# Performance work log

Hardware: AMD Instinct MI355X
Metric: run time of the kernel (lower is better)

The kernel has to match this reference:

```python
import jax, jax.numpy as jnp
import numpy as np

HIDDEN = 1024
HEADS = 16
HEAD_DIM = HIDDEN // HEADS


def setup_inputs() -> dict:
    key = jax.random.key(0)
    ks = jax.random.split(key, 9)
    s = 1.0 / np.sqrt(HIDDEN)
    x = jax.random.normal(ks[0], (2, 2048, HIDDEN), dtype=jnp.float32)
    Wq = jax.random.uniform(ks[1], (HIDDEN, HIDDEN), jnp.float32, -s, s)
    bq = jax.random.uniform(ks[2], (HIDDEN,), jnp.float32, -s, s)
    Wk = jax.random.uniform(ks[3], (HIDDEN, HIDDEN), jnp.float32, -s, s)
    bk = jax.random.uniform(ks[4], (HIDDEN,), jnp.float32, -s, s)
    Wv = jax.random.uniform(ks[5], (HIDDEN, HIDDEN), jnp.float32, -s, s)
    bv = jax.random.uniform(ks[6], (HIDDEN,), jnp.float32, -s, s)
    Wo = jax.random.uniform(ks[7], (HIDDEN, HIDDEN), jnp.float32, -s, s)
    bo = jax.random.uniform(ks[8], (HIDDEN,), jnp.float32, -s, s)
    return {"x": x, "Wq": Wq, "bq": bq, "Wk": Wk, "bk": bk,
            "Wv": Wv, "bv": bv, "Wo": Wo, "bo": bo}


def reference(x, Wq, bq, Wk, bk, Wv, bv, Wo, bo):
    bs, seq_len, _ = x.shape
    # projections; weights stored as (in, out) so y = x @ W + b
    def proj(W, b):
        y = x @ W + b  # [bs, seq, hidden]
        return y.reshape(bs, seq_len, HEADS, HEAD_DIM).transpose(0, 2, 1, 3)  # [bs, h, seq, hd]
    q = proj(Wq, bq)
    k = proj(Wk, bk)
    v = proj(Wv, bv)
    scale = 1.0 / jnp.sqrt(jnp.float32(HEAD_DIM))
    scores = jnp.einsum('bhqd,bhkd->bhqk', q, k) * scale  # [bs, h, seq, seq]
    attn = jax.nn.softmax(scores, axis=-1)
    ctx = jnp.einsum('bhqk,bhkd->bhqd', attn, v)
    ctx = ctx.transpose(0, 2, 1, 3).reshape(bs, seq_len, HIDDEN)
    return ctx @ Wo + bo
```

## Files before the change

### kernel.cpp

```cpp
#include <hip/hip_runtime.h>
#include <hip/hip_bf16.h>

#define HDN 1024
#define NH  16
#define DH  64
#define NB  2
#define SQL 2048
#define MT  (NB*SQL)

using bf16 = __hip_bfloat16;
typedef __attribute__((ext_vector_type(8))) short s16x8;
typedef __attribute__((ext_vector_type(4))) float f32x4;
typedef __attribute__((ext_vector_type(16))) float f32x16;
typedef unsigned int u32;

#define QSC 0.18033688011112042f

__device__ __forceinline__ void gload_lds16(const void* g, void* l) {
  __builtin_amdgcn_global_load_lds((const __attribute__((address_space(1))) void*)g,
                                   (__attribute__((address_space(3))) void*)l, 16, 0, 0);
}

__device__ __forceinline__ unsigned short bfb(float f) {
  union { __hip_bfloat16 h; unsigned short u; } c;
  c.h = __float2bfloat16(f);
  return c.u;
}

__device__ __forceinline__ u32 cvtpk(float lo, float hi) {
  u32 r;
  asm("v_cvt_pk_bf16_f32 %0, %1, %2" : "=v"(r) : "v"(lo), "v"(hi));
  return r;
}

__device__ __forceinline__ void pl32swap(u32& a, u32& b) {
  asm("v_permlane32_swap_b32 %0, %1" : "+v"(a), "+v"(b));
}

__global__ __launch_bounds__(256) void k_cvt_x(const float* __restrict__ x, bf16* __restrict__ xb) {
  int i = (blockIdx.x * 256 + threadIdx.x) * 8;
  float4 a = *(const float4*)(x + i);
  float4 b = *(const float4*)(x + i + 4);
  union { unsigned short u[8]; uint4 v; } o;
  o.u[0]=bfb(a.x); o.u[1]=bfb(a.y); o.u[2]=bfb(a.z); o.u[3]=bfb(a.w);
  o.u[4]=bfb(b.x); o.u[5]=bfb(b.y); o.u[6]=bfb(b.z); o.u[7]=bfb(b.w);
  *(uint4*)((unsigned short*)xb + i) = o.v;
}

__global__ __launch_bounds__(256) void k_trw(const float* __restrict__ Wq, const float* __restrict__ Wk,
                                             const float* __restrict__ Wv, const float* __restrict__ Wo,
                                             bf16* __restrict__ WqkvT, bf16* __restrict__ WoT) {
  __shared__ float tile[64][65];
  int z = blockIdx.z;
  const float* W = (z==0)?Wq:(z==1)?Wk:(z==2)?Wv:Wo;
  bf16* Wt = (z<3) ? (WqkvT + (size_t)z*HDN*HDN) : WoT;
  int r0 = blockIdx.y*64, c0 = blockIdx.x*64;
  int t = threadIdx.x, tr = t>>4, tc = (t&15)*4;
  #pragma unroll
  for (int p=0;p<4;p++){
    int r = p*16+tr;
    float4 v = *(const float4*)(W + (size_t)(r0+r)*HDN + c0 + tc);
    tile[r][tc]=v.x; tile[r][tc+1]=v.y; tile[r][tc+2]=v.z; tile[r][tc+3]=v.w;
  }
  __syncthreads();
  #pragma unroll
  for (int p=0;p<4;p++){
    int o = p*16+tr;
    union { unsigned short u[4]; ushort4 v; } pk;
    #pragma unroll
    for (int j=0;j<4;j++) pk.u[j] = bfb(tile[tc+j][o]);
    *(ushort4*)((unsigned short*)Wt + (size_t)(c0+o)*HDN + r0 + tc) = pk.v;
  }
}

template<int MODE>
__global__ __launch_bounds__(256,2) void k_gemm(
    const bf16* __restrict__ A, const bf16* __restrict__ B,
    const float* __restrict__ b0, const float* __restrict__ b1, const float* __restrict__ b2,
    bf16* __restrict__ oq, bf16* __restrict__ ok, bf16* __restrict__ ovt, float* __restrict__ oo) {
  constexpr int KD = 1024;
  __shared__ __align__(16) bf16 As[128*64];
  __shared__ __align__(16) bf16 Bs[128*64];
  int tid = threadIdx.x, lane = tid&63, wave = tid>>6;
  int g = lane>>4, lr = lane&15;
  int m0 = blockIdx.y*128, n0 = blockIdx.x*128;
  int wm = (wave>>1)*64, wn = (wave&1)*64;
  f32x4 acc[4][4] = {};
  for (int k0=0; k0<KD; k0+=64) {
    #pragma unroll
    for (int i=0;i<4;i++){
      int seg = wave*4+i;
      int flat = seg*64 + lane;
      int row = flat>>3, ch = flat&7;
      gload_lds16(A + (size_t)(m0+row)*KD + k0 + ch*8, (char*)As + seg*1024);
      gload_lds16(B + (size_t)(n0+row)*KD + k0 + ch*8, (char*)Bs + seg*1024);
    }
    __syncthreads();
    #pragma unroll
    for (int kk=0;kk<2;kk++){
      s16x8 af[4], bfg[4];
      #pragma unroll
      for (int mi=0;mi<4;mi++)
        af[mi] = *(const s16x8*)((const char*)As + (wm+mi*16+lr)*128 + kk*64 + g*16);
      #pragma unroll
      for (int ni=0;ni<4;ni++)
        bfg[ni] = *(const s16x8*)((const char*)Bs + (wn+ni*16+lr)*128 + kk*64 + g*16);
      #pragma unroll
      for (int mi=0;mi<4;mi++)
        #pragma unroll
        for (int ni=0;ni<4;ni++)
          acc[mi][ni] = __builtin_amdgcn_mfma_f32_16x16x32_bf16(af[mi], bfg[ni], acc[mi][ni], 0,0,0);
    }
    __syncthreads();
  }
  if (MODE == 0) {
    int proj = n0 >> 10;
    const float* bias = (proj==0)?b0:(proj==1)?b1:b2;
    bf16* oqk = (proj==0)?oq:ok;
    float qscale = (proj==0) ? QSC : 1.0f;
    #pragma unroll
    for (int ni=0;ni<4;ni++){
      int n = n0 + wn + ni*16 + lr;
      int wi = n & 1023;
      int h = wi>>6, d = wi&63;
      float bv = bias[wi];
      #pragma unroll
      for (int mi=0;mi<4;mi++){
        #pragma unroll
        for (int r=0;r<4;r++){
          int m = m0 + wm + mi*16 + g*4 + r;
          int b = m>>11, s = m&2047;
          float v = (acc[mi][ni][r] + bv) * qscale;
          if (proj<2) oqk[((size_t)((b*NH+h)*SQL + s))*DH + d] = __float2bfloat16(v);
          else        ovt[((size_t)((b*NH+h)*DH  + d))*SQL + s] = __float2bfloat16(v);
        }
      }
    }
  } else {
    #pragma unroll
    for (int ni=0;ni<4;ni++){
      int n = n0 + wn + ni*16 + lr;
      float bv = b0[n];
      #pragma unroll
      for (int mi=0;mi<4;mi++)
        #pragma unroll
        for (int r=0;r<4;r++){
          int m = m0 + wm + mi*16 + g*4 + r;
          oo[(size_t)m*HDN + n] = acc[mi][ni][r] + bv;
        }
    }
  }
}

__global__ __launch_bounds__(512,4) void k_attn(
    const bf16* __restrict__ Q, const bf16* __restrict__ K, const bf16* __restrict__ Vt,
    bf16* __restrict__ ctx) {
  __shared__ __align__(16) char sm[2][2][16384];
  int bh = blockIdx.x & 31, qt = blockIdx.x >> 5;
  int b = bh >> 4, h = bh & 15;
  int tid = threadIdx.x;
  int kc = tid >> 8, tl = tid & 255;
  int w4 = tl >> 6;
  int lane = tid & 63;
  int cl = lane & 31, hi = lane >> 5;
  const char* Kc = (const char*)(K  + (size_t)bh*SQL*DH);
  const char* Vc = (const char*)(Vt + (size_t)bh*DH*SQL);
  const bf16* Qb = Q + (size_t)bh*SQL*DH;

  int L0 = tl*16, L1 = 4096 + tl*16;
  int r0 = L0>>7, c0 = (L0&127) ^ ((r0&7)<<4);
  int r1 = L1>>7, c1 = (L1&127) ^ ((r1&7)<<4);
  size_t kOff0 = (size_t)r0*128  + c0, kOff1 = (size_t)r1*128  + c1;
  size_t vOff0 = (size_t)r0*4096 + c0, vOff1 = (size_t)r1*4096 + c1;

  int swz = (cl&7)<<4;
  int cswz0 = (0*32 + hi*16) ^ swz;
  int cswz1 = (1*32 + hi*16) ^ swz;
  int cswz2 = (2*32 + hi*16) ^ swz;
  int cswz3 = (3*32 + hi*16) ^ swz;
  int rbase0 = cl*128;
  int rbase1 = (32+cl)*128;

  int q0 = qt*128 + w4*32;
  s16x8 qf[4];
  #pragma unroll
  for (int ds=0; ds<4; ++ds)
    qf[ds] = *(const s16x8*)((const char*)Qb + (size_t)(q0+cl)*128 + ds*32 + hi*16);

  s16x8 onef;
  #pragma unroll
  for (int i=0;i<8;i++) onef[i] = (short)0x3F80;

  f32x16 ca0 = {}, ca1 = {}, lacc = {};

  auto STAGE = [&](int bb, int t){
    int k0 = kc*1024 + t*64;
    char* bK = &sm[kc][bb][0]; char* bV = bK + 8192;
    gload_lds16(Kc + (size_t)k0*128 + kOff0, bK + w4*1024);
    gload_lds16(Kc + (size_t)k0*128 + kOff1, bK + 4096 + w4*1024);
    gload_lds16(Vc + (size_t)k0*2   + vOff0, bV + w4*1024);
    gload_lds16(Vc + (size_t)k0*2   + vOff1, bV + 4096 + w4*1024);
  };

  STAGE(0, 0);
  __syncthreads();

  for (int t=0; t<16; ++t){
    int cur = t & 1;
    if (t < 15) STAGE(cur^1, t+1);
    const char* bK = &sm[kc][cur][0];
    const char* bV = bK + 8192;

    f32x16 s0 = {}, s1 = {};
    {
      s16x8 k00 = *(const s16x8*)(bK + rbase0 + cswz0);
      s16x8 k10 = *(const s16x8*)(bK + rbase1 + cswz0);
      s0 = __builtin_amdgcn_mfma_f32_32x32x16_bf16(k00, qf[0], s0, 0,0,0);
      s1 = __builtin_amdgcn_mfma_f32_32x32x16_bf16(k10, qf[0], s1, 0,0,0);
      s16x8 k01 = *(const s16x8*)(bK + rbase0 + cswz1);
      s16x8 k11 = *(const s16x8*)(bK + rbase1 + cswz1);
      s0 = __builtin_amdgcn_mfma_f32_32x32x16_bf16(k01, qf[1], s0, 0,0,0);
      s1 = __builtin_amdgcn_mfma_f32_32x32x16_bf16(k11, qf[1], s1, 0,0,0);
      s16x8 k02 = *(const s16x8*)(bK + rbase0 + cswz2);
      s16x8 k12 = *(const s16x8*)(bK + rbase1 + cswz2);
      s0 = __builtin_amdgcn_mfma_f32_32x32x16_bf16(k02, qf[2], s0, 0,0,0);
      s1 = __builtin_amdgcn_mfma_f32_32x32x16_bf16(k12, qf[2], s1, 0,0,0);
      s16x8 k03 = *(const s16x8*)(bK + rbase0 + cswz3);
      s16x8 k13 = *(const s16x8*)(bK + rbase1 + cswz3);
      s0 = __builtin_amdgcn_mfma_f32_32x32x16_bf16(k03, qf[3], s0, 0,0,0);
      s1 = __builtin_amdgcn_mfma_f32_32x32x16_bf16(k13, qf[3], s1, 0,0,0);
    }

    s16x8 pf[4];
    #pragma unroll
    for (int kb=0; kb<2; ++kb){
      float e[16];
      #pragma unroll
      for (int i=0;i<16;i++) e[i] = exp2f(kb ? s1[i] : s0[i]);
      u32 w00=cvtpk(e[0],e[1]),   w01=cvtpk(e[2],e[3]);
      u32 w10=cvtpk(e[4],e[5]),   w11=cvtpk(e[6],e[7]);
      u32 w20=cvtpk(e[8],e[9]),   w21=cvtpk(e[10],e[11]);
      u32 w30=cvtpk(e[12],e[13]), w31=cvtpk(e[14],e[15]);
      pl32swap(w00, w10);
      pl32swap(w01, w11);
      pl32swap(w20, w30);
      pl32swap(w21, w31);
      union { u32 u[4]; s16x8 v; } A, B;
      A.u[0]=w00; A.u[1]=w01; A.u[2]=w10; A.u[3]=w11;
      B.u[0]=w20; B.u[1]=w21; B.u[2]=w30; B.u[3]=w31;
      pf[kb*2]   = A.v;
      pf[kb*2+1] = B.v;
    }

    {
      s16x8 v00 = *(const s16x8*)(bV + rbase0 + cswz0);
      s16x8 v10 = *(const s16x8*)(bV + rbase1 + cswz0);
      ca0 = __builtin_amdgcn_mfma_f32_32x32x16_bf16(v00, pf[0], ca0, 0,0,0);
      ca1 = __builtin_amdgcn_mfma_f32_32x32x16_bf16(v10, pf[0], ca1, 0,0,0);
      lacc = __builtin_amdgcn_mfma_f32_32x32x16_bf16(onef, pf[0], lacc, 0,0,0);
      s16x8 v01 = *(const s16x8*)(bV + rbase0 + cswz1);
      s16x8 v11 = *(const s16x8*)(bV + rbase1 + cswz1);
      ca0 = __builtin_amdgcn_mfma_f32_32x32x16_bf16(v01, pf[1], ca0, 0,0,0);
      ca1 = __builtin_amdgcn_mfma_f32_32x32x16_bf16(v11, pf[1], ca1, 0,0,0);
      lacc = __builtin_amdgcn_mfma_f32_32x32x16_bf16(onef, pf[1], lacc, 0,0,0);
      s16x8 v02 = *(const s16x8*)(bV + rbase0 + cswz2);
      s16x8 v12 = *(const s16x8*)(bV + rbase1 + cswz2);
      ca0 = __builtin_amdgcn_mfma_f32_32x32x16_bf16(v02, pf[2], ca0, 0,0,0);
      ca1 = __builtin_amdgcn_mfma_f32_32x32x16_bf16(v12, pf[2], ca1, 0,0,0);
      lacc = __builtin_amdgcn_mfma_f32_32x32x16_bf16(onef, pf[2], lacc, 0,0,0);
      s16x8 v03 = *(const s16x8*)(bV + rbase0 + cswz3);
      s16x8 v13 = *(const s16x8*)(bV + rbase1 + cswz3);
      ca0 = __builtin_amdgcn_mfma_f32_32x32x16_bf16(v03, pf[3], ca0, 0,0,0);
      ca1 = __builtin_amdgcn_mfma_f32_32x32x16_bf16(v13, pf[3], ca1, 0,0,0);
      lacc = __builtin_amdgcn_mfma_f32_32x32x16_bf16(onef, pf[3], lacc, 0,0,0);
    }
    __syncthreads();
  }

  float lrow = lacc[0];

  char*  base = &sm[0][0][0];
  float* lb   = (float*)(base + 16384);
  float* o2b  = (float*)(base + 32768);
  char*  cb   = base;

  __syncthreads();
  if (kc == 1) {
    if (!hi) lb[w4*32+cl] = lrow;
    #pragma unroll
    for (int db=0; db<2; ++db)
      #pragma unroll
      for (int r=0; r<16; ++r){
        int d = db*32 + (r&3) + 8*(r>>2) + 4*hi;
        o2b[w4*2048 + d*32 + cl] = db ? ca1[r] : ca0[r];
      }
  }
  __syncthreads();
  if (kc == 0) {
    float inv = 1.f / (lrow + lb[w4*32+cl]);
    int row = w4*32 + cl;
    int rswz = (row&7)<<4;
    #pragma unroll
    for (int db=0; db<2; ++db){
      #pragma unroll
      for (int r=0; r<16; r+=2){
        int d = db*32 + (r&3) + 8*(r>>2) + 4*hi;
        float va = ((db?ca1[r]:ca0[r])     + o2b[w4*2048 + d*32     + cl]) * inv;
        float vb = ((db?ca1[r+1]:ca0[r+1]) + o2b[w4*2048 + (d+1)*32 + cl]) * inv;
        *(u32*)(cb + row*128 + ((d*2) ^ rswz)) = cvtpk(va, vb);
      }
    }
  }
  __syncthreads();
  if (kc == 0) {
    #pragma unroll
    for (int i=0;i<4;i++){
      int flat = i*256 + tl, orow = flat>>3, ch = flat&7;
      s16x8 cv = *(const s16x8*)(cb + orow*128 + ((ch*16) ^ ((orow&7)<<4)));
      *(s16x8*)(ctx + (size_t)(b*SQL + qt*128 + orow)*HDN + h*DH + ch*8) = cv;
    }
  }
}

extern "C" void kernel_launch(void* const* d_in, const int* in_sizes, int n_in,
                              void* d_out, int out_size, void* d_ws, size_t ws_size,
                              hipStream_t stream) {
  const float* x  = (const float*)d_in[0];
  const float* Wq = (const float*)d_in[1];
  const float* bq = (const float*)d_in[2];
  const float* Wk = (const float*)d_in[3];
  const float* bk = (const float*)d_in[4];
  const float* Wv = (const float*)d_in[5];
  const float* bv = (const float*)d_in[6];
  const float* Wo = (const float*)d_in[7];
  const float* bo = (const float*)d_in[8];
  char* ws = (char*)d_ws;
  bf16* xb    = (bf16*)(ws);
  bf16* WqkvT = (bf16*)(ws + ((size_t)8<<20));
  bf16* WoT   = (bf16*)(ws + ((size_t)14<<20));
  bf16* Qg    = (bf16*)(ws + ((size_t)16<<20));
  bf16* Kg    = (bf16*)(ws + ((size_t)24<<20));
  bf16* Vtg   = (bf16*)(ws + ((size_t)32<<20));
  bf16* Ctx   = (bf16*)(ws + ((size_t)40<<20));
  float* out  = (float*)d_out;

  k_cvt_x<<<2048, 256, 0, stream>>>(x, xb);
  k_trw<<<dim3(16,16,4), 256, 0, stream>>>(Wq, Wk, Wv, Wo, WqkvT, WoT);
  k_gemm<0><<<dim3(24,32), 256, 0, stream>>>(xb, WqkvT, bq, bk, bv, Qg, Kg, Vtg, nullptr);
  k_attn<<<512, 512, 0, stream>>>(Qg, Kg, Vtg, Ctx);
  k_gemm<1><<<dim3(8,32), 256, 0, stream>>>(Ctx, WoT, bo, nullptr, nullptr,
                                            nullptr, nullptr, nullptr, out);
}
```

Before: 207.9 us.

## Stage V-transpose epilogue through LDS, remap GEMM blocks, prioritize attention MFMA

```diff
diff --git a/kernel.cpp b/kernel.cpp
--- a/kernel.cpp
+++ b/kernel.cpp
@@ -79,11 +79,18 @@
     const float* __restrict__ b0, const float* __restrict__ b1, const float* __restrict__ b2,
     bf16* __restrict__ oq, bf16* __restrict__ ok, bf16* __restrict__ ovt, float* __restrict__ oo) {
   constexpr int KD = 1024;
-  __shared__ __align__(16) bf16 As[128*64];
-  __shared__ __align__(16) bf16 Bs[128*64];
+  __shared__ __align__(16) char smem[34816];
+  bf16* As = (bf16*)smem;
+  bf16* Bs = (bf16*)(smem + 16384);
   int tid = threadIdx.x, lane = tid&63, wave = tid>>6;
   int g = lane>>4, lr = lane&15;
-  int m0 = blockIdx.y*128, n0 = blockIdx.x*128;
+
+  int lin = blockIdx.y * gridDim.x + blockIdx.x;
+  int nwg = gridDim.x * gridDim.y;
+  int wg  = (lin & 7) * (nwg >> 3) + (lin >> 3);
+  int bx  = wg % gridDim.x, by = wg / gridDim.x;
+
+  int m0 = by*128, n0 = bx*128;
   int wm = (wave>>1)*64, wn = (wave&1)*64;
   f32x4 acc[4][4] = {};
   for (int k0=0; k0<KD; k0+=64) {
@@ -115,25 +122,53 @@
   }
   if (MODE == 0) {
     int proj = n0 >> 10;
-    const float* bias = (proj==0)?b0:(proj==1)?b1:b2;
-    bf16* oqk = (proj==0)?oq:ok;
-    float qscale = (proj==0) ? QSC : 1.0f;
-    #pragma unroll
-    for (int ni=0;ni<4;ni++){
-      int n = n0 + wn + ni*16 + lr;
-      int wi = n & 1023;
-      int h = wi>>6, d = wi&63;
-      float bv = bias[wi];
-      #pragma unroll
-      for (int mi=0;mi<4;mi++){
+    if (proj < 2) {
+      const float* bias = (proj==0)?b0:b1;
+      bf16* oqk = (proj==0)?oq:ok;
+      float qscale = (proj==0) ? QSC : 1.0f;
+      #pragma unroll
+      for (int ni=0;ni<4;ni++){
+        int n = n0 + wn + ni*16 + lr;
+        int wi = n & 1023;
+        int h = wi>>6, d = wi&63;
+        float bv = bias[wi];
         #pragma unroll
-        for (int r=0;r<4;r++){
-          int m = m0 + wm + mi*16 + g*4 + r;
-          int b = m>>11, s = m&2047;
-          float v = (acc[mi][ni][r] + bv) * qscale;
-          if (proj<2) oqk[((size_t)((b*NH+h)*SQL + s))*DH + d] = __float2bfloat16(v);
-          else        ovt[((size_t)((b*NH+h)*DH  + d))*SQL + s] = __float2bfloat16(v);
+        for (int mi=0;mi<4;mi++){
+          #pragma unroll
+          for (int r=0;r<4;r++){
+            int m = m0 + wm + mi*16 + g*4 + r;
+            int b = m>>11, s = m&2047;
+            float v = (acc[mi][ni][r] + bv) * qscale;
+            oqk[((size_t)((b*NH+h)*SQL + s))*DH + d] = __float2bfloat16(v);
+          }
         }
+      }
+    } else {
+      #pragma unroll
+      for (int ni=0;ni<4;ni++){
+        int nl = wn + ni*16 + lr;
+        float bv = b2[(n0 & 1023) + nl];
+        #pragma unroll
+        for (int mi=0;mi<4;mi++){
+          #pragma unroll
+          for (int rp=0; rp<4; rp+=2){
+            int ml = wm + mi*16 + g*4 + rp;
+            u32 pkd = (u32)bfb(acc[mi][ni][rp] + bv) | ((u32)bfb(acc[mi][ni][rp+1] + bv) << 16);
+            *(u32*)(smem + nl*272 + ml*2) = pkd;
+          }
+        }
+      }
+      __syncthreads();
+      int bb = m0 >> 11;
+      #pragma unroll
+      for (int it=0; it<8; ++it){
+        int flat = it*256 + tid;
+        int row = flat>>4, chk = flat&15;
+        s16x8 val = *(const s16x8*)(smem + row*272 + chk*16);
+        int wi = (n0 & 1023) + row;
+        int hh = wi>>6, dd = wi&63;
+        int ss = (m0 & 2047) + chk*8;
+        *(s16x8*)(ovt + ((size_t)((bb*NH+hh)*DH + dd))*SQL + ss) = val;
       }
     }
   } else {
@@ -212,6 +247,7 @@
     const char* bV = bK + 8192;
 
     f32x16 s0 = {}, s1 = {};
+    __builtin_amdgcn_s_setprio(1);
     {
       s16x8 k00 = *(const s16x8*)(bK + rbase0 + cswz0);
       s16x8 k10 = *(const s16x8*)(bK + rbase1 + cswz0);
@@ -230,6 +266,7 @@
       s0 = __builtin_amdgcn_mfma_f32_32x32x16_bf16(k03, qf[3], s0, 0,0,0);
       s1 = __builtin_amdgcn_mfma_f32_32x32x16_bf16(k13, qf[3], s1, 0,0,0);
     }
+    __builtin_amdgcn_s_setprio(0);
 
     s16x8 pf[4];
     #pragma unroll
@@ -252,6 +289,7 @@
       pf[kb*2+1] = B.v;
     }
 
+    __builtin_amdgcn_s_setprio(1);
     {
       s16x8 v00 = *(const s16x8*)(bV + rbase0 + cswz0);
       s16x8 v10 = *(const s16x8*)(bV + rbase1 + cswz0);
@@ -274,6 +312,7 @@
       ca1 = __builtin_amdgcn_mfma_f32_32x32x16_bf16(v13, pf[3], ca1, 0,0,0);
       lacc = __builtin_amdgcn_mfma_f32_32x32x16_bf16(onef, pf[3], lacc, 0,0,0);
     }
+    __builtin_amdgcn_s_setprio(0);
     __syncthreads();
   }
 
```

After: 197.6 us. -5.0%, faster.
